# Performance work log

Measured on AMD Instinct MI355X. Metric: run time of the kernel, lower is better.

## Reference

```python
import jax, jax.numpy as jnp
import numpy as np

I_DIM = 20000        # item (node) count; emb_mat has I_DIM+1 rows
EMB_DIM = 128        # input embedding dim
D_DIM = 128          # hidden (scaled) dim
N_EDGES = 640000     # number of (src, dst) edges


def setup_inputs() -> dict:
    key = jax.random.key(0)
    k1, k2, k3, k4 = jax.random.split(key, 4)
    emb_mat = jax.random.normal(k1, (I_DIM + 1, EMB_DIM), dtype=jnp.float32)
    # edges must be sorted by source node (column 0) so that the original
    # tf.repeat(segment_sums, bincount(src)) trick is well-defined.
    edge = jax.random.randint(k2, (N_EDGES, 2), 0, I_DIM + 1, dtype=jnp.int64)
    order = jnp.argsort(edge[:, 0])
    edge = edge[order]
    W_scale = jax.random.normal(k3, (EMB_DIM, D_DIM), dtype=jnp.float32) * 0.05
    b_scale = jnp.zeros((D_DIM,), dtype=jnp.float32)
    W_att = jax.random.normal(k4, (2 * D_DIM, 1), dtype=jnp.float32) * 0.05
    b_att = jnp.zeros((1,), dtype=jnp.float32)
    return {"emb_mat": emb_mat, "edge": edge, "W_scale": W_scale,
            "b_scale": b_scale, "W_att": W_att, "b_att": b_att}


def reference(emb_mat, edge, W_scale, b_scale, W_att, b_att):
    num_segments = emb_mat.shape[0]          # i_dim + 1
    seg = edge[:, 0]                         # source nodes (segment ids), [E]

    # gather both endpoints, scale: [E, 2, emb] -> [E, 2, d]
    edge_emb = emb_mat[edge] @ W_scale + b_scale
    E = edge_emb.shape[0]
    # attention logit per edge from concatenated endpoint features
    att = (edge_emb.reshape(E, -1) @ W_att + b_att)[:, 0]   # [E]
    att = jax.nn.leaky_relu(att, negative_slope=0.2)
    scores = jnp.exp(att - 1.0)                              # exp(att - ones)

    # manual segment softmax over edges grouped by source node
    score_sum = jax.ops.segment_sum(scores, seg, num_segments=num_segments)
    score_norm = scores / score_sum[seg]                     # [E]

    # scale all node embeddings once, gather destination features
    item_scaled = emb_mat @ W_scale + b_scale                # [N, d]
    items = item_scaled[edge[:, 1]]                          # [E, d]

    agg = jax.ops.segment_sum(score_norm[:, None] * items, seg,
                              num_segments=num_segments)     # [N, d]
    return jax.nn.sigmoid(agg)
```

## Files before the change

### kernel.cpp

```cpp
#include <hip/hip_runtime.h>
#include <math.h>

#define NSEG 20001
#define EMB  128
#define NE   640000

#define SCALE_BLOCKS 313
#define BOUNDS_BLOCKS 2500
#define LDSL 129

__device__ __forceinline__ float dot4(float4 a, float4 b) {
    return a.x*b.x + a.y*b.y + a.z*b.z + a.w*b.w;
}

#define FMA4(acc, s, b) { acc.x += (s)*(b).x; acc.y += (s)*(b).y; acc.z += (s)*(b).z; acc.w += (s)*(b).w; }

__device__ __forceinline__ unsigned f2bf(float x) {
    unsigned u = __float_as_uint(x);
    return (u + 0x7fffu + ((u >> 16) & 1u)) >> 16;
}

__global__ __launch_bounds__(256) void prep_kernel(
    const float* __restrict__ emb, const float* __restrict__ W,
    const float* __restrict__ bsc, const float* __restrict__ Watt,
    const int* __restrict__ edge,
    unsigned short* __restrict__ tab,
    float* __restrict__ a_src, float* __restrict__ a_dst,
    int* __restrict__ seg_start, int* __restrict__ dst)
{
    const int tid = threadIdx.x;
    if (blockIdx.x >= SCALE_BLOCKS) {
        int e = (blockIdx.x - SCALE_BLOCKS) * 256 + tid;
        int2 p = ((const int2*)edge)[e];
        dst[e] = p.y;
        int sp = __shfl_up(p.x, 1);
        if ((tid & 63) == 0) sp = (e == 0) ? -1 : edge[2*e - 2];
        for (int t = sp + 1; t <= p.x; ++t) seg_start[t] = e;
        if (e == NE - 1) {
            for (int t = p.x + 1; t <= NSEG; ++t) seg_start[t] = NE;
        }
        return;
    }

    __shared__ float emb_s[64 * LDSL];
    const int r0 = blockIdx.x * 64;

    const float4* embg4 = (const float4*)emb;
    const int gmax = NSEG * 32 - 1;
    #pragma unroll
    for (int j = 0; j < 8; ++j) {
        int idx = tid + j * 256;
        int row = idx >> 5, f4 = idx & 31;
        int g = r0 * 32 + idx;
        float4 v = embg4[g <= gmax ? g : gmax];
        float* p = &emb_s[row * LDSL + f4 * 4];
        p[0] = v.x; p[1] = v.y; p[2] = v.z; p[3] = v.w;
    }
    __syncthreads();

    const int cg   = tid & 15;
    const int rowb = (tid >> 4) * 4;

    float4 accA[4] = {{0,0,0,0},{0,0,0,0},{0,0,0,0},{0,0,0,0}};
    float4 accB[4] = {{0,0,0,0},{0,0,0,0},{0,0,0,0},{0,0,0,0}};
    const float4* Wg4 = (const float4*)W;

    #pragma unroll 4
    for (int k = 0; k < EMB; ++k) {
        float4 w0 = Wg4[k*32 + cg*2];
        float4 w1 = Wg4[k*32 + cg*2 + 1];
        float a0 = emb_s[(rowb+0)*LDSL + k];
        float a1 = emb_s[(rowb+1)*LDSL + k];
        float a2 = emb_s[(rowb+2)*LDSL + k];
        float a3 = emb_s[(rowb+3)*LDSL + k];
        FMA4(accA[0], a0, w0); FMA4(accB[0], a0, w1);
        FMA4(accA[1], a1, w0); FMA4(accB[1], a1, w1);
        FMA4(accA[2], a2, w0); FMA4(accB[2], a2, w1);
        FMA4(accA[3], a3, w0); FMA4(accB[3], a3, w1);
    }

    const float4 bsA = *(const float4*)&bsc[cg*8];
    const float4 bsB = *(const float4*)&bsc[cg*8 + 4];
    const float4 wsA = *(const float4*)&Watt[cg*8];
    const float4 wsB = *(const float4*)&Watt[cg*8 + 4];
    const float4 wdA = *(const float4*)&Watt[EMB + cg*8];
    const float4 wdB = *(const float4*)&Watt[EMB + cg*8 + 4];

    #pragma unroll
    for (int r = 0; r < 4; ++r) {
        float4 A = accA[r], B = accB[r];
        A.x += bsA.x; A.y += bsA.y; A.z += bsA.z; A.w += bsA.w;
        B.x += bsB.x; B.y += bsB.y; B.z += bsB.z; B.w += bsB.w;
        const int row = r0 + rowb + r;

        if (row < NSEG) {
            uint4 pkt;
            pkt.x = f2bf(A.x) | (f2bf(A.y) << 16);
            pkt.y = f2bf(A.z) | (f2bf(A.w) << 16);
            pkt.z = f2bf(B.x) | (f2bf(B.y) << 16);
            pkt.w = f2bf(B.z) | (f2bf(B.w) << 16);
            ((uint4*)tab)[row * 16 + cg] = pkt;
        }

        float ps = dot4(A, wsA) + dot4(B, wsB);
        float pd = dot4(A, wdA) + dot4(B, wdB);
        #pragma unroll
        for (int off = 8; off >= 1; off >>= 1) {
            ps += __shfl_xor(ps, off);
            pd += __shfl_xor(pd, off);
        }
        if (cg == 0 && row < NSEG) { a_src[row] = ps; a_dst[row] = pd; }
    }
}

__device__ __forceinline__ float bf_lo(unsigned u) { return __uint_as_float(u << 16); }
__device__ __forceinline__ float bf_hi(unsigned u) { return __uint_as_float(u & 0xffff0000u); }
__device__ __forceinline__ float bcastf(float v, int j) {
    return __uint_as_float(__builtin_amdgcn_readlane(__float_as_uint(v), j));
}

__global__ __launch_bounds__(256) void agg_kernel(
    const int* __restrict__ dst, const float* __restrict__ a_src,
    const float* __restrict__ a_dst, const float* __restrict__ b_att,
    const int* __restrict__ seg_start, const unsigned int* __restrict__ tab32,
    float* __restrict__ out)
{
    const int half = blockIdx.x & 1;
    const int wid  = (blockIdx.x >> 1) * 4 + (threadIdx.x >> 6);
    if (wid >= NSEG) return;
    const int lane = threadIdx.x & 63;
    const int sub  = lane >> 5;
    const int dw   = lane & 31;
    const unsigned int* tabl = tab32 + half * 32 + dw;

    const int s0 = seg_start[wid];
    const int s1 = seg_start[wid + 1];
    const float aS = a_src[wid] + b_att[0];

    float accx = 0.f, accy = 0.f, ssum = 0.f;

    for (int cb = s0; cb < s1; cb += 64) {
        int n = s1 - cb; if (n > 64) n = 64;
        int e = cb + lane;
        int dmine = 0; float sc = 0.f;
        if (lane < n) {
            dmine = dst[e] << 6;
            float att = aS + a_dst[dmine >> 6];
            att = att > 0.f ? att : 0.2f * att;
            sc  = expf(att - 1.f);
        }
        ssum += sc;

        int j = 0;
        for (; j + 15 < n; j += 16) {
            #pragma unroll
            for (int p = 0; p < 8; ++p) {
                float wa = bcastf(sc, j + 2*p);
                float wb = bcastf(sc, j + 2*p + 1);
                int   da = __builtin_amdgcn_readlane(dmine, j + 2*p);
                int   db = __builtin_amdgcn_readlane(dmine, j + 2*p + 1);
                float w = sub ? wb : wa;
                int   d = sub ? db : da;
                unsigned u = tabl[d];
                accx += w * bf_lo(u);
                accy += w * bf_hi(u);
            }
        }
        for (; j < n; j += 2) {
            float wa = bcastf(sc, j);
            int   da = __builtin_amdgcn_readlane(dmine, j);
            float wb = 0.f; int db = da;
            if (j + 1 < n) {
                wb = bcastf(sc, j + 1);
                db = __builtin_amdgcn_readlane(dmine, j + 1);
            }
            float w = sub ? wb : wa;
            int   d = sub ? db : da;
            unsigned u = tabl[d];
            accx += w * bf_lo(u);
            accy += w * bf_hi(u);
        }
    }

    #pragma unroll
    for (int off = 32; off >= 1; off >>= 1) ssum += __shfl_xor(ssum, off);

    accx += __shfl_xor(accx, 32);
    accy += __shfl_xor(accy, 32);

    const float inv = (s1 > s0) ? 1.f / ssum : 0.f;
    if (lane < 32) {
        float ox = 1.f / (1.f + expf(-accx * inv));
        float oy = 1.f / (1.f + expf(-accy * inv));
        *(float2*)&out[wid * EMB + half * 64 + 2 * dw] = make_float2(ox, oy);
    }
}

extern "C" void kernel_launch(void* const* d_in, const int* in_sizes, int n_in,
                              void* d_out, int out_size, void* d_ws, size_t ws_size,
                              hipStream_t stream) {
    const float* emb  = (const float*)d_in[0];
    const int*   edge = (const int*)  d_in[1];
    const float* W    = (const float*)d_in[2];
    const float* bsc  = (const float*)d_in[3];
    const float* Watt = (const float*)d_in[4];
    const float* batt = (const float*)d_in[5];
    float* out = (float*)d_out;

    unsigned short* tab = (unsigned short*)d_ws;
    float* a_src = (float*)(tab + (size_t)NSEG * EMB);
    float* a_dst = a_src + NSEG;
    int*   seg_start = (int*)(a_dst + NSEG);
    int*   dstc = seg_start + NSEG + 3;

    prep_kernel<<<SCALE_BLOCKS + BOUNDS_BLOCKS, 256, 0, stream>>>(
        emb, W, bsc, Watt, edge, tab, a_src, a_dst, seg_start, dstc);
    agg_kernel<<<2 * ((NSEG + 3) / 4), 256, 0, stream>>>(
        dstc, a_src, a_dst, batt, seg_start, (const unsigned int*)tab, out);
}
```

Baseline: 125.3 us.

## Quantize scaled item table to int8 with per-row scale and gather full rows per wave

Stores the scaled item table as int8 with a per-row absmax scale instead of bf16, folding the scale into the per-edge softmax weight. Each wave now aggregates all 128 columns of a node, four per lane, so the grid halves and the per-edge index loads and exp work are no longer duplicated across two column halves. This cuts gather bytes per edge in half but adds integer unpacking and conversion work and lowers the precision of the aggregated features.

Result: faster. 114.6 us (-8.6%).

```diff
diff --git a/kernel.cpp b/kernel.cpp
--- a/kernel.cpp
+++ b/kernel.cpp
@@ -15,16 +15,16 @@
 
 #define FMA4(acc, s, b) { acc.x += (s)*(b).x; acc.y += (s)*(b).y; acc.z += (s)*(b).z; acc.w += (s)*(b).w; }
 
-__device__ __forceinline__ unsigned f2bf(float x) {
-    unsigned u = __float_as_uint(x);
-    return (u + 0x7fffu + ((u >> 16) & 1u)) >> 16;
+__device__ __forceinline__ unsigned q8(float v, float inv) {
+    return (unsigned)(__float2int_rn(v * inv)) & 255u;
 }
 
 __global__ __launch_bounds__(256) void prep_kernel(
     const float* __restrict__ emb, const float* __restrict__ W,
     const float* __restrict__ bsc, const float* __restrict__ Watt,
     const int* __restrict__ edge,
-    unsigned short* __restrict__ tab,
+    signed char* __restrict__ tab8,
+    float* __restrict__ rscale,
     float* __restrict__ a_src, float* __restrict__ a_dst,
     int* __restrict__ seg_start, int* __restrict__ dst)
 {
@@ -93,13 +93,18 @@
         B.x += bsB.x; B.y += bsB.y; B.z += bsB.z; B.w += bsB.w;
         const int row = r0 + rowb + r;
 
+        float m = fmaxf(fmaxf(fmaxf(fabsf(A.x), fabsf(A.y)), fmaxf(fabsf(A.z), fabsf(A.w))),
+                        fmaxf(fmaxf(fabsf(B.x), fabsf(B.y)), fmaxf(fabsf(B.z), fabsf(B.w))));
+        #pragma unroll
+        for (int off = 1; off <= 8; off <<= 1) m = fmaxf(m, __shfl_xor(m, off));
+        const float qinv = (m > 0.f) ? 127.f / m : 0.f;
+
         if (row < NSEG) {
-            uint4 pkt;
-            pkt.x = f2bf(A.x) | (f2bf(A.y) << 16);
-            pkt.y = f2bf(A.z) | (f2bf(A.w) << 16);
-            pkt.z = f2bf(B.x) | (f2bf(B.y) << 16);
-            pkt.w = f2bf(B.z) | (f2bf(B.w) << 16);
-            ((uint4*)tab)[row * 16 + cg] = pkt;
+            int2 pkt;
+            pkt.x = (int)(q8(A.x,qinv) | (q8(A.y,qinv) << 8) | (q8(A.z,qinv) << 16) | (q8(A.w,qinv) << 24));
+            pkt.y = (int)(q8(B.x,qinv) | (q8(B.y,qinv) << 8) | (q8(B.z,qinv) << 16) | (q8(B.w,qinv) << 24));
+            ((int2*)tab8)[row * 16 + cg] = pkt;
+            if (cg == 0) rscale[row] = m * (1.f / 127.f);
         }
 
         float ps = dot4(A, wsA) + dot4(B, wsB);
@@ -113,8 +118,6 @@
     }
 }
 
-__device__ __forceinline__ float bf_lo(unsigned u) { return __uint_as_float(u << 16); }
-__device__ __forceinline__ float bf_hi(unsigned u) { return __uint_as_float(u & 0xffff0000u); }
 __device__ __forceinline__ float bcastf(float v, int j) {
     return __uint_as_float(__builtin_amdgcn_readlane(__float_as_uint(v), j));
 }
@@ -122,32 +125,33 @@
 __global__ __launch_bounds__(256) void agg_kernel(
     const int* __restrict__ dst, const float* __restrict__ a_src,
     const float* __restrict__ a_dst, const float* __restrict__ b_att,
-    const int* __restrict__ seg_start, const unsigned int* __restrict__ tab32,
-    float* __restrict__ out)
+    const float* __restrict__ rscale, const int* __restrict__ seg_start,
+    const unsigned int* __restrict__ tab32, float* __restrict__ out)
 {
-    const int half = blockIdx.x & 1;
-    const int wid  = (blockIdx.x >> 1) * 4 + (threadIdx.x >> 6);
+    const int wid = blockIdx.x * 4 + (threadIdx.x >> 6);
     if (wid >= NSEG) return;
     const int lane = threadIdx.x & 63;
     const int sub  = lane >> 5;
     const int dw   = lane & 31;
-    const unsigned int* tabl = tab32 + half * 32 + dw;
+    const unsigned int* tabl = tab32 + dw;
 
     const int s0 = seg_start[wid];
     const int s1 = seg_start[wid + 1];
     const float aS = a_src[wid] + b_att[0];
 
-    float accx = 0.f, accy = 0.f, ssum = 0.f;
+    float c0=0.f, c1=0.f, c2=0.f, c3=0.f, ssum = 0.f;
 
     for (int cb = s0; cb < s1; cb += 64) {
         int n = s1 - cb; if (n > 64) n = 64;
         int e = cb + lane;
-        int dmine = 0; float sc = 0.f;
+        int dmine = 0; float sc = 0.f, wsc = 0.f;
         if (lane < n) {
-            dmine = dst[e] << 6;
-            float att = aS + a_dst[dmine >> 6];
+            int d = dst[e];
+            dmine = d << 5;
+            float att = aS + a_dst[d];
             att = att > 0.f ? att : 0.2f * att;
             sc  = expf(att - 1.f);
+            wsc = sc * rscale[d];
         }
         ssum += sc;
 
@@ -155,44 +159,53 @@
         for (; j + 15 < n; j += 16) {
             #pragma unroll
             for (int p = 0; p < 8; ++p) {
-                float wa = bcastf(sc, j + 2*p);
-                float wb = bcastf(sc, j + 2*p + 1);
+                float wa = bcastf(wsc, j + 2*p);
+                float wb = bcastf(wsc, j + 2*p + 1);
                 int   da = __builtin_amdgcn_readlane(dmine, j + 2*p);
                 int   db = __builtin_amdgcn_readlane(dmine, j + 2*p + 1);
                 float w = sub ? wb : wa;
                 int   d = sub ? db : da;
-                unsigned u = tabl[d];
-                accx += w * bf_lo(u);
-                accy += w * bf_hi(u);
+                int u = (int)tabl[d];
+                c0 += w * (float)((u << 24) >> 24);
+                c1 += w * (float)((u << 16) >> 24);
+                c2 += w * (float)((u <<  8) >> 24);
+                c3 += w * (float)( u        >> 24);
             }
         }
         for (; j < n; j += 2) {
-            float wa = bcastf(sc, j);
+            float wa = bcastf(wsc, j);
             int   da = __builtin_amdgcn_readlane(dmine, j);
             float wb = 0.f; int db = da;
             if (j + 1 < n) {
-                wb = bcastf(sc, j + 1);
+                wb = bcastf(wsc, j + 1);
                 db = __builtin_amdgcn_readlane(dmine, j + 1);
             }
             float w = sub ? wb : wa;
             int   d = sub ? db : da;
-            unsigned u = tabl[d];
-            accx += w * bf_lo(u);
-            accy += w * bf_hi(u);
+            int u = (int)tabl[d];
+            c0 += w * (float)((u << 24) >> 24);
+            c1 += w * (float)((u << 16) >> 24);
+            c2 += w * (float)((u <<  8) >> 24);
+            c3 += w * (float)( u        >> 24);
         }
     }
 
     #pragma unroll
     for (int off = 32; off >= 1; off >>= 1) ssum += __shfl_xor(ssum, off);
 
-    accx += __shfl_xor(accx, 32);
-    accy += __shfl_xor(accy, 32);
+    c0 += __shfl_xor(c0, 32);
+    c1 += __shfl_xor(c1, 32);
+    c2 += __shfl_xor(c2, 32);
+    c3 += __shfl_xor(c3, 32);
 
     const float inv = (s1 > s0) ? 1.f / ssum : 0.f;
     if (lane < 32) {
-        float ox = 1.f / (1.f + expf(-accx * inv));
-        float oy = 1.f / (1.f + expf(-accy * inv));
-        *(float2*)&out[wid * EMB + half * 64 + 2 * dw] = make_float2(ox, oy);
+        float4 o;
+        o.x = 1.f / (1.f + expf(-c0 * inv));
+        o.y = 1.f / (1.f + expf(-c1 * inv));
+        o.z = 1.f / (1.f + expf(-c2 * inv));
+        o.w = 1.f / (1.f + expf(-c3 * inv));
+        *(float4*)&out[wid * EMB + 4 * dw] = o;
     }
 }
 
@@ -207,14 +220,15 @@
     const float* batt = (const float*)d_in[5];
     float* out = (float*)d_out;
 
-    unsigned short* tab = (unsigned short*)d_ws;
-    float* a_src = (float*)(tab + (size_t)NSEG * EMB);
+    signed char* tab8 = (signed char*)d_ws;
+    float* rscale = (float*)(tab8 + (size_t)NSEG * EMB);
+    float* a_src = rscale + NSEG;
     float* a_dst = a_src + NSEG;
     int*   seg_start = (int*)(a_dst + NSEG);
     int*   dstc = seg_start + NSEG + 3;
 
     prep_kernel<<<SCALE_BLOCKS + BOUNDS_BLOCKS, 256, 0, stream>>>(
-        emb, W, bsc, Watt, edge, tab, a_src, a_dst, seg_start, dstc);
-    agg_kernel<<<2 * ((NSEG + 3) / 4), 256, 0, stream>>>(
-        dstc, a_src, a_dst, batt, seg_start, (const unsigned int*)tab, out);
-}
+        emb, W, bsc, Watt, edge, tab8, rscale, a_src, a_dst, seg_start, dstc);
+    agg_kernel<<<(NSEG + 3) / 4, 256, 0, stream>>>(
+        dstc, a_src, a_dst, batt, rscale, seg_start, (const unsigned int*)tab8, out);
+}
```
